# Performance work log

Measured on AMD Instinct MI355X. Metric: run time of the kernel, lower is better.

Reference implementation:

```python
import jax, jax.numpy as jnp
import numpy as np

B, N, C, M = 8, 65536, 64, 64


def _build_frequency_lattice(num_modes: int) -> np.ndarray:
    candidates = []
    radius = 1
    while len(candidates) < num_modes * 2:
        for kx in range(-radius, radius + 1):
            for ky in range(-radius, radius + 1):
                if kx == 0 and ky == 0:
                    continue
                candidates.append((abs(kx) + abs(ky), kx, ky))
        radius += 1
    candidates.sort(key=lambda it: (it[0], abs(it[1]), abs(it[2]), it[1], it[2]))
    unique, seen = [], set()
    for _, kx, ky in candidates:
        if (kx, ky) in seen:
            continue
        seen.add((kx, ky))
        unique.append((kx, ky))
        if len(unique) >= num_modes:
            break
    return np.asarray(unique, dtype=np.float32)  # [M, 2]


def setup_inputs() -> dict:
    key = jax.random.key(0)
    k1, k2, k3, k4 = jax.random.split(key, 4)
    inputs = jax.random.normal(k1, (B, N, C), dtype=jnp.float32)
    coords = jax.random.uniform(k2, (B, N, 2), dtype=jnp.float32)
    scale = 1.0 / C
    # complex weight (M, C) split into real/imag float parts
    weight_re = scale * jax.random.normal(k3, (M, C), dtype=jnp.float32)
    weight_im = scale * jax.random.normal(k4, (M, C), dtype=jnp.float32)
    frequencies = jnp.asarray(_build_frequency_lattice(M))  # [M, 2]
    return {"inputs": inputs, "coords": coords, "weight_re": weight_re,
            "weight_im": weight_im, "frequencies": frequencies}


def reference(inputs, coords, weight_re, weight_im, frequencies):
    # phase: [B, N, M]
    phase = 2.0 * jnp.pi * jnp.einsum('bnc,mc->bnm', coords, frequencies)
    basis = jnp.exp(1j * phase.astype(jnp.complex64))  # [B, N, M]
    # project onto modes: [B, M, C], normalized by N
    coeffs = jnp.einsum('bnm,bnc->bmc', jnp.conj(basis), inputs.astype(jnp.complex64))
    coeffs = coeffs / N
    weight = weight_re + 1j * weight_im  # [M, C]
    mixed = coeffs * weight[None, :, :]  # [B, M, C]
    reconstructed = jnp.einsum('bnm,bmd->bnd', basis, mixed)  # [B, N, C]
    return jnp.real(reconstructed)
```

## Files before the change

kernel.cpp:

```cpp
#include <hip/hip_runtime.h>
#include <hip/hip_bf16.h>

#define BB 8
#define NN 65536
#define CC 64
#define MM 64

#define TWO_PI 6.283185307179586476925286766559f

typedef __attribute__((ext_vector_type(8))) short bf16x8;
typedef __attribute__((ext_vector_type(4))) float f32x4;
typedef unsigned int u32;
typedef unsigned short u16;

__device__ inline u32 pk_bf2(float a, float b) {
  __hip_bfloat162 h = __float22bfloat162_rn(make_float2(a, b));
  u32 r;
  __builtin_memcpy(&r, &h, 4);
  return r;
}

__device__ inline u16 sbf(float a) {
  __hip_bfloat16 h = __float2bfloat16(a);
  u16 r;
  __builtin_memcpy(&r, &h, 2);
  return r;
}

#define CH1 64
#define STEPS1 16

__global__ __launch_bounds__(256) void proj_mfma(
    const float* __restrict__ inputs,
    const float* __restrict__ coords,
    const float* __restrict__ freqs,
    float* __restrict__ partial)
{
  __shared__ __align__(16) u16 As[2][128 * 64];
  __shared__ __align__(16) u16 Xs[2][64 * 64];

  const int tid   = threadIdx.x;
  const int b     = blockIdx.x >> 6;
  const int nbase = (blockIdx.x & 63) * 1024;
  const int lane  = tid & 63;
  const int wave  = tid >> 6;
  const int l15   = lane & 15;
  const int quad  = lane >> 4;

  const int bm = tid & 63;
  const int pg = tid >> 6;
  const float fx = freqs[2 * bm];
  const float fy = freqs[2 * bm + 1];

  const int np = tid & 15;
  const int cq = tid >> 4;

  const float4* c4 = (const float4*)coords;
  const float4* x4 = (const float4*)inputs;

  float4 cpre[2][4];
  float4 xpre[2][2];

  auto load_step = [&](int s) {
#pragma unroll
    for (int g = 0; g < 2; ++g) {
      const int nb = nbase + s * 64 + (pg * 2 + g) * 8;
#pragma unroll
      for (int jj = 0; jj < 4; ++jj)
        cpre[g][jj] = c4[(size_t)(b * NN + nb + jj * 2) >> 1];
    }
#pragma unroll
    for (int half = 0; half < 2; ++half) {
      const int n = nbase + s * 64 + half * 32 + 2 * np;
      xpre[half][0] = x4[(size_t)(b * NN + n) * 16 + cq];
      xpre[half][1] = x4[(size_t)(b * NN + n + 1) * 16 + cq];
    }
  };

  auto stage_step = [&](int buf) {
#pragma unroll
    for (int g = 0; g < 2; ++g) {
      const int k8 = pg * 2 + g;
      u32 cpk[4], spk[4];
#pragma unroll
      for (int jj = 0; jj < 4; ++jj) {
        const float4 cc = cpre[g][jj];
        const float ph0 = TWO_PI * fmaf(cc.x, fx, cc.y * fy);
        const float ph1 = TWO_PI * fmaf(cc.z, fx, cc.w * fy);
        float s0, c0, s1, c1;
        __sincosf(ph0, &s0, &c0);
        __sincosf(ph1, &s1, &c1);
        cpk[jj] = pk_bf2(c0, c1);
        spk[jj] = pk_bf2(s0, s1);
      }
      *(uint4*)&As[buf][bm * 64 + ((k8 + bm) & 7) * 8] =
          make_uint4(cpk[0], cpk[1], cpk[2], cpk[3]);
      const int rs = bm + 64;
      *(uint4*)&As[buf][rs * 64 + ((k8 + rs) & 7) * 8] =
          make_uint4(spk[0], spk[1], spk[2], spk[3]);
    }
#pragma unroll
    for (int half = 0; half < 2; ++half) {
      const int k = half * 32 + 2 * np;
      const int k8 = k >> 3, koff = k & 7;
      const float* p0 = (const float*)&xpre[half][0];
      const float* p1 = (const float*)&xpre[half][1];
#pragma unroll
      for (int j = 0; j < 4; ++j) {
        const int c = cq * 4 + j;
        *(u32*)&Xs[buf][c * 64 + ((k8 + c) & 7) * 8 + koff] = pk_bf2(p0[j], p1[j]);
      }
    }
  };

  f32x4 acc[2][4];
#pragma unroll
  for (int rt = 0; rt < 2; ++rt)
#pragma unroll
    for (int ct = 0; ct < 4; ++ct) acc[rt][ct] = (f32x4){0.f, 0.f, 0.f, 0.f};

  load_step(0);
  stage_step(0);
  __syncthreads();

  for (int s = 0; s < STEPS1; ++s) {
    const int cur = s & 1;
    if (s + 1 < STEPS1) load_step(s + 1);

#pragma unroll
    for (int kk = 0; kk < 2; ++kk) {
      const int k8q = kk * 4 + quad;
      const int r0 = wave * 32 + l15;
      const int r1 = r0 + 16;
      const bf16x8 a0 = *(const bf16x8*)&As[cur][r0 * 64 + ((k8q + r0) & 7) * 8];
      const bf16x8 a1 = *(const bf16x8*)&As[cur][r1 * 64 + ((k8q + r1) & 7) * 8];
      bf16x8 bfr[4];
#pragma unroll
      for (int ct = 0; ct < 4; ++ct) {
        const int c = ct * 16 + l15;
        bfr[ct] = *(const bf16x8*)&Xs[cur][c * 64 + ((k8q + c) & 7) * 8];
      }
#pragma unroll
      for (int ct = 0; ct < 4; ++ct) {
        acc[0][ct] = __builtin_amdgcn_mfma_f32_16x16x32_bf16(a0, bfr[ct], acc[0][ct], 0, 0, 0);
        acc[1][ct] = __builtin_amdgcn_mfma_f32_16x16x32_bf16(a1, bfr[ct], acc[1][ct], 0, 0, 0);
      }
    }

    if (s + 1 < STEPS1) stage_step(1 - cur);
    __syncthreads();
  }

  float* pb = partial + (size_t)blockIdx.x * (128 * 64);
#pragma unroll
  for (int rt = 0; rt < 2; ++rt)
#pragma unroll
    for (int ct = 0; ct < 4; ++ct)
#pragma unroll
      for (int r = 0; r < 4; ++r) {
        const int mrow = wave * 32 + rt * 16 + quad * 4 + r;
        const int c = ct * 16 + l15;
        pb[mrow * 64 + c] = acc[rt][ct][r];
      }
}

__global__ __launch_bounds__(256) void mix_kernel(
    const float* __restrict__ partial,
    const float* __restrict__ wre, const float* __restrict__ wim,
    u16* __restrict__ w2t)
{
  const int idx = blockIdx.x * 256 + threadIdx.x;
  const int b = idx >> 12;
  const int m = (idx >> 6) & 63;
  const int c = idx & 63;
  const float* pb = partial + (size_t)b * CH1 * 8192;
  float gre = 0.f, gim = 0.f;
  for (int k = 0; k < CH1; ++k) {
    gre += pb[(size_t)k * 8192 + m * 64 + c];
    gim += pb[(size_t)k * 8192 + (64 + m) * 64 + c];
  }
  const float invN = 1.0f / (float)NN;
  const float wr = wre[m * 64 + c], wi = wim[m * 64 + c];
  u16* wb_ = w2t + (size_t)b * 64 * 128;
  wb_[c * 128 + m]      = sbf((gre * wr + gim * wi) * invN);
  wb_[c * 128 + 64 + m] = sbf((gim * wr - gre * wi) * invN);
}

#define TILES2 8

__global__ __launch_bounds__(256) void recon_mfma(
    const float* __restrict__ coords,
    const u16* __restrict__ w2t,
    const float* __restrict__ freqs,
    float* __restrict__ out)
{
  __shared__ __align__(16) u16 Ps[2][128 * 128];
  __shared__ float sfx[64], sfy[64];

  const int tid   = threadIdx.x;
  const int b     = blockIdx.x >> 6;
  const int nbase = (blockIdx.x & 63) * 1024;
  const int lane  = tid & 63;
  const int wave  = tid >> 6;
  const int l15   = lane & 15;
  const int quad  = lane >> 4;

  if (tid < 64) { sfx[tid] = freqs[2 * tid]; sfy[tid] = freqs[2 * tid + 1]; }

  bf16x8 wb[4][4];
#pragma unroll
  for (int kc = 0; kc < 4; ++kc)
#pragma unroll
    for (int ct = 0; ct < 4; ++ct)
      wb[kc][ct] = *(const bf16x8*)&w2t[((size_t)b * 64 + ct * 16 + l15) * 128 +
                                        kc * 32 + quad * 8];
  __syncthreads();

  const int p  = tid & 127;
  const int mg = (tid >> 7) * 32;
  const float2* c2 = (const float2*)coords;

  auto stage_tile = [&](int buf, float2 cc) {
#pragma unroll
    for (int g = 0; g < 4; ++g) {
      u32 cpk[4], spk[4];
#pragma unroll
      for (int jj = 0; jj < 4; ++jj) {
        const int m = mg + g * 8 + jj * 2;
        const float ph0 = TWO_PI * fmaf(cc.x, sfx[m], cc.y * sfy[m]);
        const float ph1 = TWO_PI * fmaf(cc.x, sfx[m + 1], cc.y * sfy[m + 1]);
        float s0, c0, s1, c1;
        __sincosf(ph0, &s0, &c0);
        __sincosf(ph1, &s1, &c1);
        cpk[jj] = pk_bf2(c0, c1);
        spk[jj] = pk_bf2(s0, s1);
      }
      const int k8c = (mg >> 3) + g;
      const int k8s = k8c + 8;
      *(uint4*)&Ps[buf][p * 128 + ((k8c + p) & 15) * 8] =
          make_uint4(cpk[0], cpk[1], cpk[2], cpk[3]);
      *(uint4*)&Ps[buf][p * 128 + ((k8s + p) & 15) * 8] =
          make_uint4(spk[0], spk[1], spk[2], spk[3]);
    }
  };

  float2 cpre = c2[(size_t)b * NN + nbase + p];
  stage_tile(0, cpre);
  __syncthreads();

  for (int t = 0; t < TILES2; ++t) {
    const int cur = t & 1;
    const int n0 = nbase + t * 128;

    float2 cnext;
    if (t + 1 < TILES2) cnext = c2[(size_t)b * NN + n0 + 128 + p];

    f32x4 acc[2][4];
#pragma unroll
    for (int rt = 0; rt < 2; ++rt)
#pragma unroll
      for (int ct = 0; ct < 4; ++ct) acc[rt][ct] = (f32x4){0.f, 0.f, 0.f, 0.f};

#pragma unroll
    for (int kc = 0; kc < 4; ++kc) {
      const int k8q = kc * 4 + quad;
      const int r0 = wave * 32 + l15;
      const int r1 = r0 + 16;
      const bf16x8 a0 = *(const bf16x8*)&Ps[cur][r0 * 128 + ((k8q + r0) & 15) * 8];
      const bf16x8 a1 = *(const bf16x8*)&Ps[cur][r1 * 128 + ((k8q + r1) & 15) * 8];
#pragma unroll
      for (int ct = 0; ct < 4; ++ct) {
        acc[0][ct] = __builtin_amdgcn_mfma_f32_16x16x32_bf16(a0, wb[kc][ct], acc[0][ct], 0, 0, 0);
        acc[1][ct] = __builtin_amdgcn_mfma_f32_16x16x32_bf16(a1, wb[kc][ct], acc[1][ct], 0, 0, 0);
      }
    }

    if (t + 1 < TILES2) stage_tile(1 - cur, cnext);

    float* ob = out + ((size_t)b * NN + n0) * 64;
#pragma unroll
    for (int rt = 0; rt < 2; ++rt)
#pragma unroll
      for (int ct = 0; ct < 4; ++ct)
#pragma unroll
        for (int r = 0; r < 4; ++r) {
          const int row = wave * 32 + rt * 16 + quad * 4 + r;
          ob[row * 64 + ct * 16 + l15] = acc[rt][ct][r];
        }

    __syncthreads();
  }
}

extern "C" void kernel_launch(void* const* d_in, const int* in_sizes, int n_in,
                              void* d_out, int out_size, void* d_ws, size_t ws_size,
                              hipStream_t stream) {
  const float* inputs = (const float*)d_in[0];
  const float* coords = (const float*)d_in[1];
  const float* wre    = (const float*)d_in[2];
  const float* wim    = (const float*)d_in[3];
  const float* freqs  = (const float*)d_in[4];
  float* out = (float*)d_out;

  float* partial = (float*)d_ws;
  u16*   w2t     = (u16*)((char*)d_ws + (size_t)BB * CH1 * 128 * 64 * 4);

  proj_mfma<<<dim3(BB * CH1), dim3(256), 0, stream>>>(inputs, coords, freqs, partial);
  mix_kernel<<<dim3(128), dim3(256), 0, stream>>>(partial, wre, wim, w2t);
  recon_mfma<<<dim3(BB * CH1), dim3(256), 0, stream>>>(coords, w2t, freqs, out);
}
```

Measured before the change: 266.3 us.

## Use hardware revolution-based sin/cos and deepen prefetch in projection and reconstruction

Replaces __sincosf on a 2π-scaled phase with fract plus the native amdgcn sin/cos instructions, which take their argument in revolutions, so the 2π multiply and range reduction are dropped. The projection kernel's thread-to-work mapping is changed so each thread handles 8 modes for one coordinate pair, with per-thread frequencies held in registers and coalesced coordinate loads. Both MFMA kernels now prefetch two steps ahead with fully unrolled loops, and the mix reduction loop is unrolled. The cost is more registers and narrower 4-byte LDS stores in the projection staging, and accuracy depends on the hardware sin/cos on the fract-reduced input.

Result: no change. 262.4 us (-1.5%).

```diff
diff --git a/kernel.cpp b/kernel.cpp
--- a/kernel.cpp
+++ b/kernel.cpp
@@ -5,8 +5,6 @@
 #define NN 65536
 #define CC 64
 #define MM 64
-
-#define TWO_PI 6.283185307179586476925286766559f
 
 typedef __attribute__((ext_vector_type(8))) short bf16x8;
 typedef __attribute__((ext_vector_type(4))) float f32x4;
@@ -25,6 +23,12 @@
   u16 r;
   __builtin_memcpy(&r, &h, 2);
   return r;
+}
+
+__device__ inline void rsc(float t, float& sn, float& cs) {
+  const float tf = __builtin_amdgcn_fractf(t);
+  sn = __builtin_amdgcn_sinf(tf);
+  cs = __builtin_amdgcn_cosf(tf);
 }
 
 #define CH1 64
@@ -47,68 +51,60 @@
   const int l15   = lane & 15;
   const int quad  = lane >> 4;
 
-  const int bm = tid & 63;
-  const int pg = tid >> 6;
-  const float fx = freqs[2 * bm];
-  const float fy = freqs[2 * bm + 1];
-
+  const int q  = tid & 31;
+  const int mg = tid >> 5;
   const int np = tid & 15;
   const int cq = tid >> 4;
 
+  float fqx[8], fqy[8];
+#pragma unroll
+  for (int mm = 0; mm < 8; ++mm) {
+    fqx[mm] = freqs[2 * (mg * 8 + mm)];
+    fqy[mm] = freqs[2 * (mg * 8 + mm) + 1];
+  }
+
   const float4* c4 = (const float4*)coords;
   const float4* x4 = (const float4*)inputs;
-
-  float4 cpre[2][4];
-  float4 xpre[2][2];
-
-  auto load_step = [&](int s) {
-#pragma unroll
-    for (int g = 0; g < 2; ++g) {
-      const int nb = nbase + s * 64 + (pg * 2 + g) * 8;
-#pragma unroll
-      for (int jj = 0; jj < 4; ++jj)
-        cpre[g][jj] = c4[(size_t)(b * NN + nb + jj * 2) >> 1];
-    }
+  const size_t cbase = ((size_t)b * NN + nbase) >> 1;
+  const size_t xbase = ((size_t)b * NN + nbase) * 16;
+
+  float4 cs_[2];
+  float4 xs_[2][4];
+
+  auto do_load = [&](int s, int slot) {
+    cs_[slot] = c4[cbase + (size_t)s * 32 + q];
 #pragma unroll
     for (int half = 0; half < 2; ++half) {
-      const int n = nbase + s * 64 + half * 32 + 2 * np;
-      xpre[half][0] = x4[(size_t)(b * NN + n) * 16 + cq];
-      xpre[half][1] = x4[(size_t)(b * NN + n + 1) * 16 + cq];
+      const int n = s * 64 + half * 32 + 2 * np;
+      xs_[slot][half * 2 + 0] = x4[xbase + (size_t)n * 16 + cq];
+      xs_[slot][half * 2 + 1] = x4[xbase + (size_t)(n + 1) * 16 + cq];
     }
   };
 
-  auto stage_step = [&](int buf) {
-#pragma unroll
-    for (int g = 0; g < 2; ++g) {
-      const int k8 = pg * 2 + g;
-      u32 cpk[4], spk[4];
-#pragma unroll
-      for (int jj = 0; jj < 4; ++jj) {
-        const float4 cc = cpre[g][jj];
-        const float ph0 = TWO_PI * fmaf(cc.x, fx, cc.y * fy);
-        const float ph1 = TWO_PI * fmaf(cc.z, fx, cc.w * fy);
-        float s0, c0, s1, c1;
-        __sincosf(ph0, &s0, &c0);
-        __sincosf(ph1, &s1, &c1);
-        cpk[jj] = pk_bf2(c0, c1);
-        spk[jj] = pk_bf2(s0, s1);
-      }
-      *(uint4*)&As[buf][bm * 64 + ((k8 + bm) & 7) * 8] =
-          make_uint4(cpk[0], cpk[1], cpk[2], cpk[3]);
-      const int rs = bm + 64;
-      *(uint4*)&As[buf][rs * 64 + ((k8 + rs) & 7) * 8] =
-          make_uint4(spk[0], spk[1], spk[2], spk[3]);
+  auto do_stage = [&](int slot, int buf) {
+    const float4 cp = cs_[slot];
+    const int k8 = q >> 2;
+    const int ko = (2 * q) & 7;
+#pragma unroll
+    for (int mm = 0; mm < 8; ++mm) {
+      const int rc = mg * 8 + mm;
+      const int rs = rc + 64;
+      float s0, c0, s1, c1;
+      rsc(fmaf(cp.x, fqx[mm], cp.y * fqy[mm]), s0, c0);
+      rsc(fmaf(cp.z, fqx[mm], cp.w * fqy[mm]), s1, c1);
+      *(u32*)&As[buf][rc * 64 + ((k8 + rc) & 7) * 8 + ko] = pk_bf2(c0, c1);
+      *(u32*)&As[buf][rs * 64 + ((k8 + rs) & 7) * 8 + ko] = pk_bf2(s0, s1);
     }
 #pragma unroll
     for (int half = 0; half < 2; ++half) {
       const int k = half * 32 + 2 * np;
-      const int k8 = k >> 3, koff = k & 7;
-      const float* p0 = (const float*)&xpre[half][0];
-      const float* p1 = (const float*)&xpre[half][1];
+      const int k8x = k >> 3, kox = k & 7;
+      const float* p0 = (const float*)&xs_[slot][half * 2 + 0];
+      const float* p1 = (const float*)&xs_[slot][half * 2 + 1];
 #pragma unroll
       for (int j = 0; j < 4; ++j) {
         const int c = cq * 4 + j;
-        *(u32*)&Xs[buf][c * 64 + ((k8 + c) & 7) * 8 + koff] = pk_bf2(p0[j], p1[j]);
+        *(u32*)&Xs[buf][c * 64 + ((k8x + c) & 7) * 8 + kox] = pk_bf2(p0[j], p1[j]);
       }
     }
   };
@@ -119,26 +115,19 @@
 #pragma unroll
     for (int ct = 0; ct < 4; ++ct) acc[rt][ct] = (f32x4){0.f, 0.f, 0.f, 0.f};
 
-  load_step(0);
-  stage_step(0);
-  __syncthreads();
-
-  for (int s = 0; s < STEPS1; ++s) {
-    const int cur = s & 1;
-    if (s + 1 < STEPS1) load_step(s + 1);
-
+  auto do_mfma = [&](int buf) {
 #pragma unroll
     for (int kk = 0; kk < 2; ++kk) {
       const int k8q = kk * 4 + quad;
       const int r0 = wave * 32 + l15;
       const int r1 = r0 + 16;
-      const bf16x8 a0 = *(const bf16x8*)&As[cur][r0 * 64 + ((k8q + r0) & 7) * 8];
-      const bf16x8 a1 = *(const bf16x8*)&As[cur][r1 * 64 + ((k8q + r1) & 7) * 8];
+      const bf16x8 a0 = *(const bf16x8*)&As[buf][r0 * 64 + ((k8q + r0) & 7) * 8];
+      const bf16x8 a1 = *(const bf16x8*)&As[buf][r1 * 64 + ((k8q + r1) & 7) * 8];
       bf16x8 bfr[4];
 #pragma unroll
       for (int ct = 0; ct < 4; ++ct) {
         const int c = ct * 16 + l15;
-        bfr[ct] = *(const bf16x8*)&Xs[cur][c * 64 + ((k8q + c) & 7) * 8];
+        bfr[ct] = *(const bf16x8*)&Xs[buf][c * 64 + ((k8q + c) & 7) * 8];
       }
 #pragma unroll
       for (int ct = 0; ct < 4; ++ct) {
@@ -146,8 +135,19 @@
         acc[1][ct] = __builtin_amdgcn_mfma_f32_16x16x32_bf16(a1, bfr[ct], acc[1][ct], 0, 0, 0);
       }
     }
-
-    if (s + 1 < STEPS1) stage_step(1 - cur);
+  };
+
+  do_load(0, 0);
+  do_load(1, 1);
+  do_stage(0, 0);
+  __syncthreads();
+
+#pragma unroll
+  for (int s = 0; s < STEPS1; ++s) {
+    const int cur = s & 1;
+    if (s + 2 < STEPS1) do_load(s + 2, cur);
+    do_mfma(cur);
+    if (s + 1 < STEPS1) do_stage(1 - cur, 1 - cur);
     __syncthreads();
   }
 
@@ -175,6 +175,7 @@
   const int c = idx & 63;
   const float* pb = partial + (size_t)b * CH1 * 8192;
   float gre = 0.f, gim = 0.f;
+#pragma unroll 8
   for (int k = 0; k < CH1; ++k) {
     gre += pb[(size_t)k * 8192 + m * 64 + c];
     gim += pb[(size_t)k * 8192 + (64 + m) * 64 + c];
@@ -207,6 +208,15 @@
 
   if (tid < 64) { sfx[tid] = freqs[2 * tid]; sfy[tid] = freqs[2 * tid + 1]; }
 
+  const int p  = tid & 127;
+  const int mg = (tid >> 7) * 32;
+  const float2* c2 = (const float2*)coords;
+  const size_t cb = (size_t)b * NN + nbase;
+
+  float2 cpre[2];
+  cpre[0] = c2[cb + p];
+  cpre[1] = c2[cb + 128 + p];
+
   bf16x8 wb[4][4];
 #pragma unroll
   for (int kc = 0; kc < 4; ++kc)
@@ -216,10 +226,6 @@
                                         kc * 32 + quad * 8];
   __syncthreads();
 
-  const int p  = tid & 127;
-  const int mg = (tid >> 7) * 32;
-  const float2* c2 = (const float2*)coords;
-
   auto stage_tile = [&](int buf, float2 cc) {
 #pragma unroll
     for (int g = 0; g < 4; ++g) {
@@ -227,11 +233,9 @@
 #pragma unroll
       for (int jj = 0; jj < 4; ++jj) {
         const int m = mg + g * 8 + jj * 2;
-        const float ph0 = TWO_PI * fmaf(cc.x, sfx[m], cc.y * sfy[m]);
-        const float ph1 = TWO_PI * fmaf(cc.x, sfx[m + 1], cc.y * sfy[m + 1]);
         float s0, c0, s1, c1;
-        __sincosf(ph0, &s0, &c0);
-        __sincosf(ph1, &s1, &c1);
+        rsc(fmaf(cc.x, sfx[m], cc.y * sfy[m]), s0, c0);
+        rsc(fmaf(cc.x, sfx[m + 1], cc.y * sfy[m + 1]), s1, c1);
         cpk[jj] = pk_bf2(c0, c1);
         spk[jj] = pk_bf2(s0, s1);
       }
@@ -244,16 +248,13 @@
     }
   };
 
-  float2 cpre = c2[(size_t)b * NN + nbase + p];
-  stage_tile(0, cpre);
+  stage_tile(0, cpre[0]);
   __syncthreads();
 
+#pragma unroll
   for (int t = 0; t < TILES2; ++t) {
     const int cur = t & 1;
-    const int n0 = nbase + t * 128;
-
-    float2 cnext;
-    if (t + 1 < TILES2) cnext = c2[(size_t)b * NN + n0 + 128 + p];
+    if (t + 2 < TILES2) cpre[cur] = c2[cb + (size_t)(t + 2) * 128 + p];
 
     f32x4 acc[2][4];
 #pragma unroll
@@ -275,9 +276,9 @@
       }
     }
 
-    if (t + 1 < TILES2) stage_tile(1 - cur, cnext);
-
-    float* ob = out + ((size_t)b * NN + n0) * 64;
+    if (t + 1 < TILES2) stage_tile(1 - cur, cpre[1 - cur]);
+
+    float* ob = out + (cb + (size_t)t * 128) * 64;
 #pragma unroll
     for (int rt = 0; rt < 2; ++rt)
 #pragma unroll
```
